# Kernel tuning notes

Measured on AMD Instinct MI355X. Metric: run time of the kernel, lower is better.

## Reference

```python
import jax, jax.numpy as jnp
import numpy as np
from jax.ops import segment_sum


def setup_inputs() -> dict:
    key = jax.random.key(0)
    ks = jax.random.split(key, 9)
    N, E, D, C = 50000, 800000, 128, 16
    s = 1.0 / np.sqrt(D)
    return {
        "x": jnp.arange(N, dtype=jnp.int64) if jax.config.jax_enable_x64 else jnp.arange(N, dtype=jnp.int32),
        "edge_index": jax.random.randint(ks[0], (2, E), 0, N, dtype=jnp.int32),
        "emb": jax.random.normal(ks[1], (N, D), jnp.float32),
        "W0": jax.random.normal(ks[2], (D, D), jnp.float32) * s,
        "b0": jax.random.normal(ks[3], (D,), jnp.float32) * 0.01,
        "W1": jax.random.normal(ks[4], (D, D), jnp.float32) * s,
        "b1": jax.random.normal(ks[5], (D,), jnp.float32) * 0.01,
        "Wc": jax.random.normal(ks[6], (D, C), jnp.float32) * s,
        "bc": jax.random.normal(ks[7], (C,), jnp.float32) * 0.01,
    }


def _gcn_layer(h, W, b, src, dst, norm, N):
    # PyG GCNConv: h' = D^{-1/2}(A+I)D^{-1/2} (h W) + b  (self-loops already in src/dst)
    h = h @ W                                   # [N, D]
    msg = h[src] * norm[:, None]                # gather + edge-normalize  [Et, D]
    return segment_sum(msg, dst, num_segments=N) + b


def reference(x, edge_index, emb, W0, b0, W1, b1, Wc, bc):
    N = emb.shape[0]
    h = emb[x]                                  # embedding lookup  [N, D]
    # add self-loops
    loops = jnp.arange(N, dtype=edge_index.dtype)
    src = jnp.concatenate([edge_index[0], loops])
    dst = jnp.concatenate([edge_index[1], loops])
    # symmetric degree normalization (deg counts incoming edges incl. self-loop)
    deg = segment_sum(jnp.ones_like(src, dtype=h.dtype), dst, num_segments=N)
    dinv = jnp.where(deg > 0, jax.lax.rsqrt(deg), 0.0)
    norm = dinv[src] * dinv[dst]                # [Et]
    h = jax.nn.relu(_gcn_layer(h, W0, b0, src, dst, norm, N))
    h = jax.nn.relu(_gcn_layer(h, W1, b1, src, dst, norm, N))
    # dropout is identity in eval mode (deterministic reference)
    return h @ Wc + bc                          # [N, num_classes]
```

## Files before the change

### kernel.cpp

```cpp
#include <hip/hip_runtime.h>
#include <hip/hip_bf16.h>

#define D 128
#define C 16
#define NBMAX 512
#define VPT 16
#define CAP 8192

typedef unsigned int uint;
typedef unsigned short ushort;
typedef __attribute__((ext_vector_type(8))) short short8;
typedef __attribute__((ext_vector_type(4))) float f32x4;

__device__ __forceinline__ uint pack_bf16(float a, float b) {
    uint ua = __float_as_uint(a);
    uint ub = __float_as_uint(b);
    ua += 0x7fffu + ((ua >> 16) & 1u);
    ub += 0x7fffu + ((ub >> 16) & 1u);
    return (ua >> 16) | (ub & 0xffff0000u);
}
__device__ __forceinline__ ushort bf1(float a) {
    uint u = __float_as_uint(a);
    u += 0x7fffu + ((u >> 16) & 1u);
    return (ushort)(u >> 16);
}
__device__ __forceinline__ float bf_lo(uint u) { return __uint_as_float(u << 16); }
__device__ __forceinline__ float bf_hi(uint u) { return __uint_as_float(u & 0xffff0000u); }

__global__ __launch_bounds__(256) void k_prep(const int* __restrict__ src,
                                              const int* __restrict__ dst,
                                              const float* __restrict__ W0,
                                              const float* __restrict__ W1,
                                              const float* __restrict__ Wc,
                                              ushort* __restrict__ Wt0,
                                              ushort* __restrict__ Wt1,
                                              ushort* __restrict__ Wct,
                                              int* __restrict__ cur,
                                              uint* __restrict__ tmp,
                                              uint* __restrict__ h16,
                                              int E, int shift, int N) {
    __shared__ int lcnt[NBMAX];
    __shared__ int lbase[NBMAX];
    int tid = threadIdx.x;
    int mask = (1 << shift) - 1;
    lcnt[tid] = 0; lcnt[tid + 256] = 0;
    __syncthreads();
    long e0 = (long)blockIdx.x * (256 * VPT);
    uint ps[VPT]; int pb[VPT];
    #pragma unroll
    for (int t = 0; t < VPT; ++t) {
        long e = e0 + t * 256 + tid;
        if (e < E) {
            int s = src[e], d = dst[e];
            int b = d >> shift;
            pb[t] = b;
            ps[t] = (uint)s | ((uint)(d & mask) << 17);
            atomicAdd(&lcnt[b], 1);
        } else pb[t] = -1;
    }
    __syncthreads();
    for (int b = tid; b < NBMAX; b += 256) {
        int c = lcnt[b];
        lbase[b] = c ? atomicAdd(&cur[b], c) : 0;
    }
    __syncthreads();
    lcnt[tid] = 0; lcnt[tid + 256] = 0;
    __syncthreads();
    #pragma unroll
    for (int t = 0; t < VPT; ++t) {
        if (pb[t] >= 0) {
            int r = atomicAdd(&lcnt[pb[t]], 1);
            int pos = lbase[pb[t]] + r;
            if (pos < CAP)
                tmp[(size_t)pb[t] * CAP + pos] = ps[t];
        }
    }

    for (int i = blockIdx.x * 256 + tid; i < D * D; i += gridDim.x * 256) {
        int n = i >> 7, k = i & 127;
        Wt0[i] = bf1(W0[k * D + n]);
        Wt1[i] = bf1(W1[k * D + n]);
    }
    for (int i = blockIdx.x * 256 + tid; i < D * C; i += gridDim.x * 256) {
        int c2 = i >> 7, k = i & 127;
        Wct[i] = bf1(Wc[k * C + c2]);
    }
    if (blockIdx.x == 0 && tid < 64) h16[(size_t)N * 64 + tid] = 0;
}

__global__ __launch_bounds__(256) void k_build(const uint* __restrict__ tmp,
                                               const int* __restrict__ cur,
                                               const int* __restrict__ x,
                                               const float* __restrict__ emb,
                                               uint* __restrict__ nodeinfo,
                                               float* __restrict__ dinv,
                                               int* __restrict__ col,
                                               uint* __restrict__ h16,
                                               int N, int shift, int NB) {
    __shared__ int   lc[256];
    __shared__ int   lrow[256];
    __shared__ int   lcur[256];
    __shared__ float lfd[256];
    int b = blockIdx.x, tid = threadIdx.x;
    int W = 1 << shift;
    if (tid < W) lc[tid] = 0;
    __syncthreads();
    int cnt = min(cur[b], CAP);
    const uint* bt = tmp + (size_t)b * CAP;
    for (int i = tid; i < cnt; i += 256)
        atomicAdd(&lc[bt[i] >> 17], 1);
    __syncthreads();
    int v0 = (b << shift) + tid;
    int degt = 0, nb8 = 0;
    if (tid < W) {
        degt = (v0 < N) ? lc[tid] + 1 : 0;
        nb8  = (degt + 7) >> 3;
        lrow[tid] = nb8;
    }
    __syncthreads();
    for (int off = 1; off < W; off <<= 1) {
        int t = 0;
        if (tid < W && tid >= off) t = lrow[tid - off];
        __syncthreads();
        if (tid < W) lrow[tid] += t;
        __syncthreads();
    }
    int bstart_base = b * (CAP / 8 + W);
    int slot0 = 0;
    if (tid < W) {
        int bstart = bstart_base + lrow[tid] - nb8;
        slot0 = bstart << 3;
        float dv = rsqrtf((float)degt);
        lrow[tid] = slot0;
        lcur[tid] = 1;
        lfd[tid]  = dv;
        if (v0 < N) {
            nodeinfo[v0] = ((uint)bstart << 8) | (uint)nb8;
            dinv[v0] = dv;
            col[slot0] = v0;
        }
    }
    __syncthreads();
    for (int i = tid; i < cnt; i += 256) {
        uint u = bt[i];
        int off = (int)(u >> 17);
        int r = atomicAdd(&lcur[off], 1);
        col[lrow[off] + r] = (int)(u & 0x1FFFFu);
    }
    __syncthreads();
    if (tid < W && v0 < N) {
        for (int i = degt; i < (nb8 << 3); ++i) col[slot0 + i] = N;
    }
    for (int idx = tid; idx < W * 16; idx += 256) {
        int row = idx >> 4;
        int j8  = idx & 15;
        int v = (b << shift) + row;
        if (v >= N) continue;
        float dv = lfd[row];
        int xr = x[v];
        const float4* e4 = (const float4*)(emb + (size_t)xr * D + j8 * 8);
        float4 a = e4[0], bb = e4[1];
        uint4 o;
        o.x = pack_bf16(a.x * dv, a.y * dv);
        o.y = pack_bf16(a.z * dv, a.w * dv);
        o.z = pack_bf16(bb.x * dv, bb.y * dv);
        o.w = pack_bf16(bb.z * dv, bb.w * dv);
        ((uint4*)(h16 + (size_t)v * 64))[j8] = o;
    }
}

template<bool FUSE>
__global__ __launch_bounds__(1024, 2) void k_fused(const uint* __restrict__ hin,
                                                   const uint* __restrict__ nodeinfo,
                                                   const int* __restrict__ col,
                                                   const float* __restrict__ dinv,
                                                   const ushort* __restrict__ Wt,
                                                   const float* __restrict__ b,
                                                   uint* __restrict__ hout16,
                                                   const ushort* __restrict__ Wct,
                                                   const float* __restrict__ bc,
                                                   float* __restrict__ outf, int N) {
    __shared__ __align__(16) ushort T[64][136];
    __shared__ int wptr;
    int tid  = threadIdx.x;
    int wv = tid >> 6, lane = tid & 63;
    long tile0 = (long)blockIdx.x * 64;

    if (tid == 0) wptr = 0;
    __syncthreads();

    for (;;) {
        int i = 0;
        if (lane == 0) i = atomicAdd(&wptr, 1);
        i = __builtin_amdgcn_readfirstlane(i);
        if (i >= 64) break;
        long v = tile0 + i;
        float ax = 0.f, ay = 0.f;
        if (v < N) {
            uint info = (uint)__builtin_amdgcn_readfirstlane((int)nodeinfo[v]);
            int e   = (int)(info >> 8) << 3;
            int nb8 = (int)(info & 255u);
            int k2 = 0;
            for (; k2 + 2 <= nb8; k2 += 2, e += 16) {
                int c[16]; uint u[16];
                #pragma unroll
                for (int t = 0; t < 16; ++t) c[t] = __builtin_amdgcn_readfirstlane(col[e + t]);
                #pragma unroll
                for (int t = 0; t < 16; ++t) u[t] = hin[(size_t)c[t] * 64 + lane];
                #pragma unroll
                for (int t = 0; t < 16; ++t) { ax += bf_lo(u[t]); ay += bf_hi(u[t]); }
            }
            if (k2 < nb8) {
                int c[8]; uint u[8];
                #pragma unroll
                for (int t = 0; t < 8; ++t) c[t] = __builtin_amdgcn_readfirstlane(col[e + t]);
                #pragma unroll
                for (int t = 0; t < 8; ++t) u[t] = hin[(size_t)c[t] * 64 + lane];
                #pragma unroll
                for (int t = 0; t < 8; ++t) { ax += bf_lo(u[t]); ay += bf_hi(u[t]); }
            }
            float dv = dinv[v];
            ax *= dv; ay *= dv;
        }
        *(uint*)&T[i][lane * 2] = pack_bf16(ax, ay);
    }
    __syncthreads();

    int rq  = wv & 3;
    int nt0 = (wv >> 2) * 2;
    int c0 = lane & 15, g = lane >> 4;

    short8 a[4];
    #pragma unroll
    for (int kk = 0; kk < 4; ++kk)
        a[kk] = *(const short8*)((const char*)&T[rq * 16 + c0][0] + kk * 64 + g * 16);
    __syncthreads();

    float dsc[4];
    #pragma unroll
    for (int j = 0; j < 4; ++j) {
        long r = tile0 + rq * 16 + g * 4 + j; if (r >= N) r = N - 1;
        dsc[j] = FUSE ? 1.f : dinv[r];
    }

    #pragma unroll
    for (int nt = nt0; nt < nt0 + 2; ++nt) {
        float bias = b[nt * 16 + c0];
        f32x4 acc = {bias, bias, bias, bias};
        const ushort* wb = Wt + (size_t)(nt * 16 + c0) * D + g * 8;
        #pragma unroll
        for (int kk = 0; kk < 4; ++kk) {
            short8 bf = *(const short8*)(wb + kk * 32);
            acc = __builtin_amdgcn_mfma_f32_16x16x32_bf16(a[kk], bf, acc, 0, 0, 0);
        }
        #pragma unroll
        for (int j = 0; j < 4; ++j)
            T[rq * 16 + g * 4 + j][nt * 16 + c0] = bf1(fmaxf(acc[j], 0.f) * dsc[j]);
    }
    __syncthreads();

    if (!FUSE) {
        int r = tid >> 4, q = tid & 15;
        long grow = tile0 + r;
        if (grow < N) {
            *(uint4*)((char*)(hout16 + grow * 64) + q * 16) =
                *(const uint4*)((const char*)&T[r][0] + q * 16);
        }
    } else if (wv < 4) {
        float biasc = bc[c0];
        f32x4 acc2 = {biasc, biasc, biasc, biasc};
        #pragma unroll
        for (int kk = 0; kk < 4; ++kk) {
            short8 ta = *(const short8*)((const char*)&T[wv * 16 + c0][0] + kk * 64 + g * 16);
            short8 wc = *(const short8*)(Wct + (size_t)c0 * D + kk * 32 + g * 8);
            acc2 = __builtin_amdgcn_mfma_f32_16x16x32_bf16(ta, wc, acc2, 0, 0, 0);
        }
        #pragma unroll
        for (int j = 0; j < 4; ++j) {
            long grow = tile0 + wv * 16 + g * 4 + j;
            if (grow < N) outf[grow * C + c0] = acc2[j];
        }
    }
}


extern "C" void kernel_launch(void* const* d_in, const int* in_sizes, int n_in,
                              void* d_out, int out_size, void* d_ws, size_t ws_size,
                              hipStream_t stream) {
    const int*   x    = (const int*)  d_in[0];
    const int*   ei   = (const int*)  d_in[1];
    const float* emb  = (const float*)d_in[2];
    const float* W0   = (const float*)d_in[3];
    const float* b0   = (const float*)d_in[4];
    const float* W1   = (const float*)d_in[5];
    const float* b1   = (const float*)d_in[6];
    const float* Wc   = (const float*)d_in[7];
    const float* bc   = (const float*)d_in[8];
    float* out = (float*)d_out;

    const int N  = in_sizes[0];
    const int E  = in_sizes[1] / 2;

    const int* src = ei;
    const int* dst = ei + E;

    int shift = 7;
    while (((N + (1 << shift) - 1) >> shift) > NBMAX) shift++;
    const int NB = (N + (1 << shift) - 1) >> shift;
    const int W  = 1 << shift;

    const size_t colCap = (size_t)NB * (CAP / 8 + W) * 8 + 64;

    char* p = (char*)d_ws;
    auto take = [&](size_t bytes) { char* q = p; p += (bytes + 255) & ~(size_t)255; return q; };
    uint*   nodeinfo = (uint*) take((size_t)N * 4);
    float*  dinv    = (float*) take((size_t)N * 4);
    int*    cur     = (int*)   take((size_t)NBMAX * 4);
    uint*   tmp     = (uint*)  take((size_t)NB * CAP * 4);
    int*    col     = (int*)   take(colCap * 4);
    ushort* Wt0     = (ushort*)take((size_t)D * D * 2);
    ushort* Wt1     = (ushort*)take((size_t)D * D * 2);
    ushort* Wct     = (ushort*)take((size_t)D * C * 2);
    uint*   hA16    = (uint*)  take((size_t)(N + 1) * 64 * 4);
    uint*   hB16    = (uint*)  take((size_t)(N + 1) * 64 * 4);

    const int BS = 256;
    const int EB = (int)(((long)E + 256 * VPT - 1) / (256 * VPT));
    const int NT = (N + 63) / 64;

    hipMemsetAsync(cur, 0, NBMAX * 4, stream);
    k_prep <<<EB, BS, 0, stream>>>(src, dst, W0, W1, Wc, Wt0, Wt1, Wct,
                                   cur, tmp, hA16, E, shift, N);
    k_build<<<NB, BS, 0, stream>>>(tmp, cur, x, emb, nodeinfo, dinv, col, hA16,
                                   N, shift, NB);

    hipMemsetAsync(hB16 + (size_t)N * 64, 0, 64 * 4, stream);

    k_fused<false><<<NT, 1024, 0, stream>>>(hA16, nodeinfo, col, dinv, Wt0, b0,
                                            hB16, nullptr, nullptr, nullptr, N);
    k_fused<true><<<NT, 1024, 0, stream>>>(hB16, nodeinfo, col, dinv, Wt1, b1,
                                           nullptr, Wct, bc, out, N);
}
```

Before: 126.8 us.

## Make fused GCN layer kernels persistent with atomic tile work queue

Converts the two fused aggregate+GEMM kernels from one block per 64-node tile to a fixed grid of 512 persistent blocks that grab tiles via a global atomic counter. Each block loops over tiles, resetting its intra-tile wave counter per tile, with an extra barrier at the end of each iteration. The aim is to smooth load imbalance from varying node degrees and to cut block launch/teardown overhead. In exchange it adds a global atomic per tile and extra synchronisation, and it fixes the grid size regardless of how many blocks the device can keep resident.

```diff
diff --git a/kernel.cpp b/kernel.cpp
--- a/kernel.cpp
+++ b/kernel.cpp
@@ -179,107 +179,117 @@
                                                    uint* __restrict__ hout16,
                                                    const ushort* __restrict__ Wct,
                                                    const float* __restrict__ bc,
-                                                   float* __restrict__ outf, int N) {
+                                                   float* __restrict__ outf,
+                                                   int* __restrict__ tileCtr,
+                                                   int N, int NT) {
     __shared__ __align__(16) ushort T[64][136];
     __shared__ int wptr;
+    __shared__ int tloc;
     int tid  = threadIdx.x;
     int wv = tid >> 6, lane = tid & 63;
-    long tile0 = (long)blockIdx.x * 64;
-
-    if (tid == 0) wptr = 0;
-    __syncthreads();
-
-    for (;;) {
-        int i = 0;
-        if (lane == 0) i = atomicAdd(&wptr, 1);
-        i = __builtin_amdgcn_readfirstlane(i);
-        if (i >= 64) break;
-        long v = tile0 + i;
-        float ax = 0.f, ay = 0.f;
-        if (v < N) {
-            uint info = (uint)__builtin_amdgcn_readfirstlane((int)nodeinfo[v]);
-            int e   = (int)(info >> 8) << 3;
-            int nb8 = (int)(info & 255u);
-            int k2 = 0;
-            for (; k2 + 2 <= nb8; k2 += 2, e += 16) {
-                int c[16]; uint u[16];
-                #pragma unroll
-                for (int t = 0; t < 16; ++t) c[t] = __builtin_amdgcn_readfirstlane(col[e + t]);
-                #pragma unroll
-                for (int t = 0; t < 16; ++t) u[t] = hin[(size_t)c[t] * 64 + lane];
-                #pragma unroll
-                for (int t = 0; t < 16; ++t) { ax += bf_lo(u[t]); ay += bf_hi(u[t]); }
-            }
-            if (k2 < nb8) {
-                int c[8]; uint u[8];
-                #pragma unroll
-                for (int t = 0; t < 8; ++t) c[t] = __builtin_amdgcn_readfirstlane(col[e + t]);
-                #pragma unroll
-                for (int t = 0; t < 8; ++t) u[t] = hin[(size_t)c[t] * 64 + lane];
-                #pragma unroll
-                for (int t = 0; t < 8; ++t) { ax += bf_lo(u[t]); ay += bf_hi(u[t]); }
-            }
-            float dv = dinv[v];
-            ax *= dv; ay *= dv;
-        }
-        *(uint*)&T[i][lane * 2] = pack_bf16(ax, ay);
-    }
-    __syncthreads();
-
+    int c0 = lane & 15, g = lane >> 4;
     int rq  = wv & 3;
     int nt0 = (wv >> 2) * 2;
-    int c0 = lane & 15, g = lane >> 4;
-
-    short8 a[4];
-    #pragma unroll
-    for (int kk = 0; kk < 4; ++kk)
-        a[kk] = *(const short8*)((const char*)&T[rq * 16 + c0][0] + kk * 64 + g * 16);
-    __syncthreads();
-
-    float dsc[4];
-    #pragma unroll
-    for (int j = 0; j < 4; ++j) {
-        long r = tile0 + rq * 16 + g * 4 + j; if (r >= N) r = N - 1;
-        dsc[j] = FUSE ? 1.f : dinv[r];
-    }
-
-    #pragma unroll
-    for (int nt = nt0; nt < nt0 + 2; ++nt) {
-        float bias = b[nt * 16 + c0];
-        f32x4 acc = {bias, bias, bias, bias};
-        const ushort* wb = Wt + (size_t)(nt * 16 + c0) * D + g * 8;
+
+    for (;;) {
+        if (tid == 0) {
+            tloc = atomicAdd(tileCtr, 1);
+            wptr = 0;
+        }
+        __syncthreads();
+        int tI = tloc;
+        if (tI >= NT) break;
+        long tile0 = (long)tI * 64;
+
+        for (;;) {
+            int i = 0;
+            if (lane == 0) i = atomicAdd(&wptr, 1);
+            i = __builtin_amdgcn_readfirstlane(i);
+            if (i >= 64) break;
+            long v = tile0 + i;
+            float ax = 0.f, ay = 0.f;
+            if (v < N) {
+                uint info = (uint)__builtin_amdgcn_readfirstlane((int)nodeinfo[v]);
+                int e   = (int)(info >> 8) << 3;
+                int nb8 = (int)(info & 255u);
+                int k2 = 0;
+                for (; k2 + 2 <= nb8; k2 += 2, e += 16) {
+                    int c[16]; uint u[16];
+                    #pragma unroll
+                    for (int t = 0; t < 16; ++t) c[t] = __builtin_amdgcn_readfirstlane(col[e + t]);
+                    #pragma unroll
+                    for (int t = 0; t < 16; ++t) u[t] = hin[(size_t)c[t] * 64 + lane];
+                    #pragma unroll
+                    for (int t = 0; t < 16; ++t) { ax += bf_lo(u[t]); ay += bf_hi(u[t]); }
+                }
+                if (k2 < nb8) {
+                    int c[8]; uint u[8];
+                    #pragma unroll
+                    for (int t = 0; t < 8; ++t) c[t] = __builtin_amdgcn_readfirstlane(col[e + t]);
+                    #pragma unroll
+                    for (int t = 0; t < 8; ++t) u[t] = hin[(size_t)c[t] * 64 + lane];
+                    #pragma unroll
+                    for (int t = 0; t < 8; ++t) { ax += bf_lo(u[t]); ay += bf_hi(u[t]); }
+                }
+                float dv = dinv[v];
+                ax *= dv; ay *= dv;
+            }
+            *(uint*)&T[i][lane * 2] = pack_bf16(ax, ay);
+        }
+        __syncthreads();
+
+        short8 a[4];
         #pragma unroll
-        for (int kk = 0; kk < 4; ++kk) {
-            short8 bf = *(const short8*)(wb + kk * 32);
-            acc = __builtin_amdgcn_mfma_f32_16x16x32_bf16(a[kk], bf, acc, 0, 0, 0);
-        }
-        #pragma unroll
-        for (int j = 0; j < 4; ++j)
-            T[rq * 16 + g * 4 + j][nt * 16 + c0] = bf1(fmaxf(acc[j], 0.f) * dsc[j]);
-    }
-    __syncthreads();
-
-    if (!FUSE) {
-        int r = tid >> 4, q = tid & 15;
-        long grow = tile0 + r;
-        if (grow < N) {
-            *(uint4*)((char*)(hout16 + grow * 64) + q * 16) =
-                *(const uint4*)((const char*)&T[r][0] + q * 16);
-        }
-    } else if (wv < 4) {
-        float biasc = bc[c0];
-        f32x4 acc2 = {biasc, biasc, biasc, biasc};
-        #pragma unroll
-        for (int kk = 0; kk < 4; ++kk) {
-            short8 ta = *(const short8*)((const char*)&T[wv * 16 + c0][0] + kk * 64 + g * 16);
-            short8 wc = *(const short8*)(Wct + (size_t)c0 * D + kk * 32 + g * 8);
-            acc2 = __builtin_amdgcn_mfma_f32_16x16x32_bf16(ta, wc, acc2, 0, 0, 0);
-        }
+        for (int kk = 0; kk < 4; ++kk)
+            a[kk] = *(const short8*)((const char*)&T[rq * 16 + c0][0] + kk * 64 + g * 16);
+        __syncthreads();
+
+        float dsc[4];
         #pragma unroll
         for (int j = 0; j < 4; ++j) {
-            long grow = tile0 + wv * 16 + g * 4 + j;
-            if (grow < N) outf[grow * C + c0] = acc2[j];
-        }
+            long r = tile0 + rq * 16 + g * 4 + j; if (r >= N) r = N - 1;
+            dsc[j] = FUSE ? 1.f : dinv[r];
+        }
+
+        #pragma unroll
+        for (int nt = nt0; nt < nt0 + 2; ++nt) {
+            float bias = b[nt * 16 + c0];
+            f32x4 acc = {bias, bias, bias, bias};
+            const ushort* wb = Wt + (size_t)(nt * 16 + c0) * D + g * 8;
+            #pragma unroll
+            for (int kk = 0; kk < 4; ++kk) {
+                short8 bf = *(const short8*)(wb + kk * 32);
+                acc = __builtin_amdgcn_mfma_f32_16x16x32_bf16(a[kk], bf, acc, 0, 0, 0);
+            }
+            #pragma unroll
+            for (int j = 0; j < 4; ++j)
+                T[rq * 16 + g * 4 + j][nt * 16 + c0] = bf1(fmaxf(acc[j], 0.f) * dsc[j]);
+        }
+        __syncthreads();
+
+        if (!FUSE) {
+            int r = tid >> 4, q = tid & 15;
+            long grow = tile0 + r;
+            if (grow < N) {
+                *(uint4*)((char*)(hout16 + grow * 64) + q * 16) =
+                    *(const uint4*)((const char*)&T[r][0] + q * 16);
+            }
+        } else if (wv < 4) {
+            float biasc = bc[c0];
+            f32x4 acc2 = {biasc, biasc, biasc, biasc};
+            #pragma unroll
+            for (int kk = 0; kk < 4; ++kk) {
+                short8 ta = *(const short8*)((const char*)&T[wv * 16 + c0][0] + kk * 64 + g * 16);
+                short8 wc = *(const short8*)(Wct + (size_t)c0 * D + kk * 32 + g * 8);
+                acc2 = __builtin_amdgcn_mfma_f32_16x16x32_bf16(ta, wc, acc2, 0, 0, 0);
+            }
+            #pragma unroll
+            for (int j = 0; j < 4; ++j) {
+                long grow = tile0 + wv * 16 + g * 4 + j;
+                if (grow < N) outf[grow * C + c0] = acc2[j];
+            }
+        }
+        __syncthreads();
     }
 }
 
@@ -315,7 +325,7 @@
     auto take = [&](size_t bytes) { char* q = p; p += (bytes + 255) & ~(size_t)255; return q; };
     uint*   nodeinfo = (uint*) take((size_t)N * 4);
     float*  dinv    = (float*) take((size_t)N * 4);
-    int*    cur     = (int*)   take((size_t)NBMAX * 4);
+    int*    cur     = (int*)   take((size_t)(NBMAX + 2) * 4);
     uint*   tmp     = (uint*)  take((size_t)NB * CAP * 4);
     int*    col     = (int*)   take(colCap * 4);
     ushort* Wt0     = (ushort*)take((size_t)D * D * 2);
@@ -327,8 +337,9 @@
     const int BS = 256;
     const int EB = (int)(((long)E + 256 * VPT - 1) / (256 * VPT));
     const int NT = (N + 63) / 64;
-
-    hipMemsetAsync(cur, 0, NBMAX * 4, stream);
+    const int PERSIST = 512;
+
+    hipMemsetAsync(cur, 0, (NBMAX + 2) * 4, stream);
     k_prep <<<EB, BS, 0, stream>>>(src, dst, W0, W1, Wc, Wt0, Wt1, Wct,
                                    cur, tmp, hA16, E, shift, N);
     k_build<<<NB, BS, 0, stream>>>(tmp, cur, x, emb, nodeinfo, dinv, col, hA16,
@@ -336,8 +347,10 @@
 
     hipMemsetAsync(hB16 + (size_t)N * 64, 0, 64 * 4, stream);
 
-    k_fused<false><<<NT, 1024, 0, stream>>>(hA16, nodeinfo, col, dinv, Wt0, b0,
-                                            hB16, nullptr, nullptr, nullptr, N);
-    k_fused<true><<<NT, 1024, 0, stream>>>(hB16, nodeinfo, col, dinv, Wt1, b1,
-                                           nullptr, Wct, bc, out, N);
-}
+    k_fused<false><<<PERSIST, 1024, 0, stream>>>(hA16, nodeinfo, col, dinv, Wt0, b0,
+                                                 hB16, nullptr, nullptr, nullptr,
+                                                 cur + NBMAX, N, NT);
+    k_fused<true><<<PERSIST, 1024, 0, stream>>>(hB16, nodeinfo, col, dinv, Wt1, b1,
+                                                nullptr, Wct, bc, out,
+                                                cur + NBMAX + 1, N, NT);
+}
```

After: 145.2 us. +14.5%, slower.
